# Kernel optimization log

Measured on AMD Instinct MI355X. Metric: run time of the kernel, lower is better.

Reference implementation:

```python
import jax, jax.numpy as jnp
import numpy as np

B, N_OCR, N_OBJ, D, H, L, DFF = 64, 64, 192, 768, 12, 4, 2048
DH = D // H
EPS = 1e-5  # torch LayerNorm default


def _ln(x, g, b):
    m = jnp.mean(x, axis=-1, keepdims=True)
    v = jnp.mean(jnp.square(x - m), axis=-1, keepdims=True)
    return (x - m) * jax.lax.rsqrt(v + EPS) * g + b


def setup_inputs():
    key = jax.random.key(0)
    ks = iter(jax.random.split(key, 32))
    s = 0.02
    f = lambda shape: jax.random.normal(next(ks), shape, jnp.float32) * s
    return {
        "ocr_feats": jax.random.normal(next(ks), (B, N_OCR, D), jnp.float32),
        "obj_feats": jax.random.normal(next(ks), (B, N_OBJ, D), jnp.float32),
        "ocr_dvs": jax.random.uniform(next(ks), (B, N_OCR, 1), jnp.float32, 0.1, 2.0),
        "obj_dvs": jax.random.uniform(next(ks), (B, N_OBJ, 1), jnp.float32, 0.1, 2.0),
        # SemanticAttentionDeFUM projections
        "sa_wq": f((D, D)), "sa_bq": jnp.zeros((D,), jnp.float32),
        "sa_wk": f((D, D)), "sa_bk": jnp.zeros((D,), jnp.float32),
        "sa_wv": f((D, D)), "sa_bv": jnp.zeros((D,), jnp.float32),
        # outer LayerNorm
        "ln0_g": jnp.ones((D,), jnp.float32), "ln0_b": jnp.zeros((D,), jnp.float32),
        # stacked TransformerEncoder layer params (post-norm, batch_first)
        "qkv_w": f((L, 3 * D, D)), "qkv_b": jnp.zeros((L, 3 * D), jnp.float32),
        "out_w": f((L, D, D)), "out_b": jnp.zeros((L, D), jnp.float32),
        "ln1_g": jnp.ones((L, D), jnp.float32), "ln1_b": jnp.zeros((L, D), jnp.float32),
        "ff1_w": f((L, DFF, D)), "ff1_b": jnp.zeros((L, DFF), jnp.float32),
        "ff2_w": f((L, D, DFF)), "ff2_b": jnp.zeros((L, D), jnp.float32),
        "ln2_g": jnp.ones((L, D), jnp.float32), "ln2_b": jnp.zeros((L, D), jnp.float32),
    }


def reference(ocr_feats, obj_feats, ocr_dvs, obj_dvs,
              sa_wq, sa_bq, sa_wk, sa_bk, sa_wv, sa_bv,
              ln0_g, ln0_b,
              qkv_w, qkv_b, out_w, out_b, ln1_g, ln1_b,
              ff1_w, ff1_b, ff2_w, ff2_b, ln2_g, ln2_b):
    num_ocr = ocr_feats.shape[1]
    x = jnp.concatenate([ocr_feats, obj_feats], axis=1)       # B,N,D
    dv = jnp.concatenate([ocr_dvs, obj_dvs], axis=1)[..., 0]  # B,N
    # vectorized cal_relative_depth_map: log(max(dv_i,dv_j)/min(dv_i,dv_j))
    R = jnp.log(jnp.maximum(dv[:, :, None], dv[:, None, :]) /
                jnp.minimum(dv[:, :, None], dv[:, None, :]))  # B,N,N
    # semantic attention: scores A and values V
    q = jnp.einsum('bnd,ed->bne', x, sa_wq) + sa_bq
    k = jnp.einsum('bnd,ed->bne', x, sa_wk) + sa_bk
    v = jnp.einsum('bnd,ed->bne', x, sa_wv) + sa_bv
    A = jnp.einsum('bqd,bkd->bqk', q, k) / jnp.sqrt(jnp.float32(D))
    att = jax.nn.softmax(A + R, axis=-1)
    h = _ln(x + jnp.einsum('bqk,bkd->bqd', att, v), ln0_g, ln0_b)

    def layer(h, p):
        qw, qb, ow, ob, l1g, l1b, f1w, f1b, f2w, f2b, l2g, l2b = p
        Bn, N, _ = h.shape
        qkv = jnp.einsum('bnd,ed->bne', h, qw) + qb            # B,N,3D
        qh, kh, vh = jnp.split(qkv, 3, axis=-1)
        qh = qh.reshape(Bn, N, H, DH).transpose(0, 2, 1, 3)
        kh = kh.reshape(Bn, N, H, DH).transpose(0, 2, 1, 3)
        vh = vh.reshape(Bn, N, H, DH).transpose(0, 2, 1, 3)
        sc = jnp.einsum('bhqd,bhkd->bhqk', qh, kh) / jnp.sqrt(jnp.float32(DH))
        o = jnp.einsum('bhqk,bhkd->bhqd', jax.nn.softmax(sc, axis=-1), vh)
        o = o.transpose(0, 2, 1, 3).reshape(Bn, N, D)
        o = jnp.einsum('bnd,ed->bne', o, ow) + ob
        h = _ln(h + o, l1g, l1b)
        ff = jnp.einsum('bnd,fd->bnf', h, f1w) + f1b
        ff = jax.nn.gelu(ff, approximate=False)  # torch 'gelu' = exact erf gelu
        ff = jnp.einsum('bnf,df->bnd', ff, f2w) + f2b
        h = _ln(h + ff, l2g, l2b)
        return h, None

    h, _ = jax.lax.scan(layer, h, (qkv_w, qkv_b, out_w, out_b,
                                   ln1_g, ln1_b, ff1_w, ff1_b,
                                   ff2_w, ff2_b, ln2_g, ln2_b))
    return h[:, :num_ocr, :]
```

## Files before the change

kernel.cpp:

```cpp
#include <hip/hip_runtime.h>

typedef unsigned short u16;
typedef __bf16 bf16_t;
typedef bf16_t bf16x8 __attribute__((ext_vector_type(8)));
typedef float f32x4 __attribute__((ext_vector_type(4)));
typedef unsigned int u32x4 __attribute__((ext_vector_type(4)));
typedef u16 u16x4 __attribute__((ext_vector_type(4)));

#define GL_LDS16(gp, lp)                                              \
  __builtin_amdgcn_global_load_lds(                                   \
      (const __attribute__((address_space(1))) void*)(gp),            \
      (__attribute__((address_space(3))) void*)(lp), 16, 0, 0)

__device__ __forceinline__ u16 f2bf(float f) {
  unsigned u = __builtin_bit_cast(unsigned, f);
  u += 0x7fff + ((u >> 16) & 1);
  return (u16)(u >> 16);
}
__device__ __forceinline__ float bf2f(u16 h) {
  unsigned u = ((unsigned)h) << 16;
  return __builtin_bit_cast(float, u);
}
__device__ __forceinline__ float wredSum(float v) {
#pragma unroll
  for (int m = 32; m; m >>= 1) v += __shfl_xor(v, m);
  return v;
}

__global__ __launch_bounds__(512, 2) void gemm3r(
    const u16* __restrict__ A, const u16* __restrict__ B,
    const float* __restrict__ bias, u16* __restrict__ C,
    int K, int N, int gx, int act, int tstore) {
  extern __shared__ __align__(16) char sm[];
  const int tid = threadIdx.x;
  const int l = tid & 63, w = tid >> 6, lg = l >> 4, li = l & 15;
  const int wr = w >> 2, wc = w & 3;

  int bid = blockIdx.x;
  int G = gx >> 3;
  int xcd = bid & 7, loc = bid >> 3;
  int mt = xcd * G + (loc % G), nt = loc / G;

  const u16* Ab = A + (long)mt * 256 * K;
  const u16* Bb = B + (long)nt * 256 * K;

  const long saoff = (long)(tid >> 2) * K + (((tid & 3) ^ ((tid >> 3) & 3)) << 3);
  const long rowK128 = (long)128 * K;
  const int t16 = tid * 16;

#define STAGE_A3(bi_, kt_)                                             \
  do {                                                                 \
    const u16* gp_ = Ab + saoff + ((long)(kt_) << 5);                  \
    char* lb_ = sm + (bi_) * 32768;                                    \
    GL_LDS16(gp_, lb_ + t16);                                          \
    GL_LDS16(gp_ + rowK128, lb_ + 8192 + t16);                         \
  } while (0)
#define STAGE_B3(bi_, kt_)                                             \
  do {                                                                 \
    const u16* gp_ = Bb + saoff + ((long)(kt_) << 5);                  \
    char* lb_ = sm + (bi_) * 32768 + 16384;                            \
    GL_LDS16(gp_, lb_ + t16);                                          \
    GL_LDS16(gp_ + rowK128, lb_ + 8192 + t16);                         \
  } while (0)

#define VM8 asm volatile("s_waitcnt vmcnt(8)" ::: "memory")
#define VM4 asm volatile("s_waitcnt vmcnt(4)" ::: "memory")
#define VM0 asm volatile("s_waitcnt vmcnt(0)" ::: "memory")

  int aof[2][4], bof[4];
#pragma unroll
  for (int hi = 0; hi < 2; ++hi)
#pragma unroll
    for (int f = 0; f < 4; ++f) {
      int ra = wr * 128 + hi * 64 + f * 16 + li;
      aof[hi][f] = ra * 64 + ((lg ^ ((ra >> 1) & 3)) << 4);
    }
#pragma unroll
  for (int f = 0; f < 4; ++f) {
    int rb = wc * 64 + f * 16 + li;
    bof[f] = 16384 + rb * 64 + ((lg ^ ((rb >> 1) & 3)) << 4);
  }

  f32x4 acc[8][4] = {};

  const int NT = K >> 5;
  STAGE_B3(0, 0); STAGE_A3(0, 0);
  STAGE_B3(1, 1); STAGE_A3(1, 1);
  STAGE_B3(2, 2); STAGE_A3(2, 2);

  for (int s = 0; s < NT; ++s) {
    const int bi = s & 3, bi3 = (s + 3) & 3;
    const char* ab = sm + bi * 32768;
    if (s < NT - 2) VM8; else if (s == NT - 2) VM4; else VM0;
    __builtin_amdgcn_s_barrier();
    asm volatile("" ::: "memory");
    if (s <= NT - 4) STAGE_B3(bi3, s + 3);
    bf16x8 afr[4], bfr[4];
#pragma unroll
    for (int f = 0; f < 4; ++f) {
      afr[f] = __builtin_bit_cast(bf16x8, *(const u32x4*)(ab + aof[0][f]));
      bfr[f] = __builtin_bit_cast(bf16x8, *(const u32x4*)(ab + bof[f]));
    }
    __builtin_amdgcn_s_setprio(1);
#pragma unroll
    for (int fi = 0; fi < 4; ++fi)
#pragma unroll
      for (int fj = 0; fj < 4; ++fj)
        acc[fi][fj] = __builtin_amdgcn_mfma_f32_16x16x32_bf16(afr[fi], bfr[fj], acc[fi][fj], 0, 0, 0);
    __builtin_amdgcn_s_setprio(0);
    if (s <= NT - 4) STAGE_A3(bi3, s + 3);
    bf16x8 ag[4];
#pragma unroll
    for (int f = 0; f < 4; ++f)
      ag[f] = __builtin_bit_cast(bf16x8, *(const u32x4*)(ab + aof[1][f]));
    __builtin_amdgcn_s_setprio(1);
#pragma unroll
    for (int fi = 0; fi < 4; ++fi)
#pragma unroll
      for (int fj = 0; fj < 4; ++fj)
        acc[4 + fi][fj] = __builtin_amdgcn_mfma_f32_16x16x32_bf16(ag[fi], bfr[fj], acc[4 + fi][fj], 0, 0, 0);
    __builtin_amdgcn_s_setprio(0);
  }

  long row0 = (long)mt * 256 + wr * 128;
  int col0 = nt * 256 + wc * 64;
#pragma unroll
  for (int fi = 0; fi < 8; ++fi) {
#pragma unroll
    for (int fj = 0; fj < 4; ++fj) {
      int c = col0 + fj * 16 + li;
      float bv = bias ? bias[c] : 0.f;
#pragma unroll
      for (int r = 0; r < 4; ++r) {
        float v = acc[fi][fj][r] + bv;
        if (act) v = 0.5f * v * (1.f + erff(v * 0.70710678118f));
        long row = row0 + fi * 16 + lg * 4 + r;
        long idx = tstore ? ((row >> 8) * 196608 + (long)c * 256 + (row & 255))
                          : (row * (long)N + c);
        C[idx] = f2bf(v);
      }
    }
  }
#undef STAGE_A3
#undef STAGE_B3
#undef VM8
#undef VM4
#undef VM0
}

__global__ __launch_bounds__(256) void gemm_bt(
    const u16* __restrict__ A, const u16* __restrict__ B,
    const float* __restrict__ bias, const float* __restrict__ logdv,
    float* __restrict__ Cf, u16* __restrict__ Cb,
    int K, int ldc, long sA, long sB, long sC, float alpha, int act, int tstore) {
  __shared__ __align__(16) u16 As[2][128 * 32];
  __shared__ __align__(16) u16 Bs[2][128 * 32];
  int tid = threadIdx.x, w = tid >> 6, l = tid & 63, lg = l >> 4, li = l & 15;
  int wr = w >> 1, wc = w & 1;
  long bz = blockIdx.z;
  const u16* Ab = A + bz * sA + (long)blockIdx.x * 128 * K;
  const u16* Bb = B + bz * sB + (long)blockIdx.y * 128 * K;

  int sr = tid >> 2, ss = tid & 3;
  long ga0 = (long)sr * K + ((ss ^ ((sr >> 1) & 3)) << 3);
  long gstep = (long)K << 6;

  int aoff[4], boff[4];
#pragma unroll
  for (int i = 0; i < 4; ++i) {
    int ra = wr * 64 + i * 16 + li;
    aoff[i] = ra * 64 + ((lg ^ ((ra >> 1) & 3)) << 4);
    int rb = wc * 64 + i * 16 + li;
    boff[i] = rb * 64 + ((lg ^ ((rb >> 1) & 3)) << 4);
  }

  f32x4 acc[4][4] = {};
  int wb = w * 1024;

  GL_LDS16(Ab + ga0, (char*)As + wb);
  GL_LDS16(Ab + ga0 + gstep, (char*)As + 4096 + wb);
  GL_LDS16(Bb + ga0, (char*)Bs + wb);
  GL_LDS16(Bb + ga0 + gstep, (char*)Bs + 4096 + wb);
  __syncthreads();

  int T = K >> 5;
  int bsel = 0;
  for (int kt = 0; kt < T; ++kt) {
    if (kt + 1 < T) {
      long ko = (long)(kt + 1) << 5;
      char* an = (char*)As + (bsel ^ 1) * 8192;
      char* bn = (char*)Bs + (bsel ^ 1) * 8192;
      GL_LDS16(Ab + ga0 + ko, an + wb);
      GL_LDS16(Ab + ga0 + gstep + ko, an + 4096 + wb);
      GL_LDS16(Bb + ga0 + ko, bn + wb);
      GL_LDS16(Bb + ga0 + gstep + ko, bn + 4096 + wb);
    }
    char* ac = (char*)As + bsel * 8192;
    char* bc = (char*)Bs + bsel * 8192;
    bf16x8 af[4], bq[4];
#pragma unroll
    for (int i = 0; i < 4; ++i) {
      af[i] = __builtin_bit_cast(bf16x8, *(const u32x4*)(ac + aoff[i]));
      bq[i] = __builtin_bit_cast(bf16x8, *(const u32x4*)(bc + boff[i]));
    }
#pragma unroll
    for (int i = 0; i < 4; ++i)
#pragma unroll
      for (int j = 0; j < 4; ++j)
        acc[i][j] = __builtin_amdgcn_mfma_f32_16x16x32_bf16(af[i], bq[j], acc[i][j], 0, 0, 0);
    __syncthreads();
    bsel ^= 1;
  }

  long row0 = (long)blockIdx.x * 128 + wr * 64;
  int col0 = blockIdx.y * 128 + wc * 64;
  float* cf = Cf ? Cf + bz * sC : (float*)0;
  u16* cb = Cb ? Cb + bz * sC : (u16*)0;
  const float* ldv = logdv ? logdv + bz * 256 : (const float*)0;
#pragma unroll
  for (int i = 0; i < 4; ++i) {
    long rb0 = row0 + i * 16 + lg * 4;
#pragma unroll
    for (int j = 0; j < 4; ++j) {
      int c = col0 + j * 16 + li;
      float bv = bias ? bias[c] : 0.f;
      float lj = ldv ? ldv[c] : 0.f;
#pragma unroll
      for (int r = 0; r < 4; ++r) {
        float v = acc[i][j][r] * alpha + bv;
        if (ldv) v += fabsf(ldv[rb0 + r] - lj);
        if (act) v = 0.5f * v * (1.f + erff(v * 0.70710678118f));
        long row = rb0 + r;
        long idx = tstore ? ((row >> 8) * 196608 + (long)c * 256 + (row & 255))
                          : (row * ldc + c);
        if (cf) cf[idx] = v;
        if (cb) cb[idx] = f2bf(v);
      }
    }
  }
}

__global__ __launch_bounds__(256) void mha_k(const u16* __restrict__ qkv, u16* __restrict__ obf) {
  __shared__ __align__(16) u16 Ks[256 * 64];
  __shared__ __align__(16) u16 Vt[64 * 256];
  int b = blockIdx.y;
  int h = blockIdx.x >> 2, qt = blockIdx.x & 3;
  int tid = threadIdx.x, w = tid >> 6, l = tid & 63, lg = l >> 4, li = l & 15;
  const u16* kb_ = qkv + (long)b * 256 * 2304 + 768 + h * 64;
  const u16* vb_ = qkv + (long)b * 256 * 2304 + 1536 + h * 64;
#pragma unroll
  for (int it = 0; it < 8; ++it) {
    int c = it * 256 + tid; int n = c >> 3, sl = c & 7;
    u32x4 d = *(const u32x4*)(kb_ + (long)n * 2304 + sl * 8);
    *(u32x4*)((char*)Ks + n * 128 + ((sl ^ (n & 7)) << 4)) = d;
  }
#pragma unroll
  for (int it = 0; it < 8; ++it) {
    int c = it * 256 + tid; int n = c >> 3, sl = c & 7;
    u32x4 dv = *(const u32x4*)(vb_ + (long)n * 2304 + sl * 8);
    const u16* pe = (const u16*)&dv;
#pragma unroll
    for (int j = 0; j < 8; ++j) {
      int dd = sl * 8 + j;
      *(u16*)((char*)Vt + dd * 512 + (((n >> 3) ^ (dd & 7)) << 4) + (n & 7) * 2) = pe[j];
    }
  }
  __syncthreads();

  long qrow = (long)b * 256 + qt * 64 + w * 16 + li;
  const u16* qp = qkv + qrow * 2304 + h * 64;
  bf16x8 qf0 = __builtin_bit_cast(bf16x8, *(const u32x4*)(qp + lg * 8));
  bf16x8 qf1 = __builtin_bit_cast(bf16x8, *(const u32x4*)(qp + 32 + lg * 8));

  f32x4 sacc[16] = {};
#pragma unroll
  for (int jt = 0; jt < 16; ++jt) {
    int j = jt * 16 + li;
    u32x4 k0 = *(const u32x4*)((char*)Ks + j * 128 + ((lg ^ (j & 7)) << 4));
    u32x4 k1 = *(const u32x4*)((char*)Ks + j * 128 + (((4 + lg) ^ (j & 7)) << 4));
    sacc[jt] = __builtin_amdgcn_mfma_f32_16x16x32_bf16(qf0, __builtin_bit_cast(bf16x8, k0), sacc[jt], 0, 0, 0);
    sacc[jt] = __builtin_amdgcn_mfma_f32_16x16x32_bf16(qf1, __builtin_bit_cast(bf16x8, k1), sacc[jt], 0, 0, 0);
  }
#pragma unroll
  for (int jt = 0; jt < 16; ++jt) sacc[jt] = sacc[jt] * 0.125f;

  float rinv[4];
#pragma unroll
  for (int r = 0; r < 4; ++r) {
    float m = -1e30f;
#pragma unroll
    for (int jt = 0; jt < 16; ++jt) m = fmaxf(m, sacc[jt][r]);
#pragma unroll
    for (int mk = 1; mk < 16; mk <<= 1) m = fmaxf(m, __shfl_xor(m, mk));
    float s = 0.f;
#pragma unroll
    for (int jt = 0; jt < 16; ++jt) { float e = __expf(sacc[jt][r] - m); sacc[jt][r] = e; s += e; }
#pragma unroll
    for (int mk = 1; mk < 16; mk <<= 1) s += __shfl_xor(s, mk);
    rinv[r] = 1.f / s;
  }
  __syncthreads();
  char* Ps = (char*)Ks + w * 8192;
#pragma unroll
  for (int jt = 0; jt < 16; ++jt) {
    int j = jt * 16 + li;
#pragma unroll
    for (int r = 0; r < 4; ++r) {
      int i = lg * 4 + r;
      *(u16*)(Ps + i * 512 + (((j >> 3) ^ (i & 7)) << 4) + (j & 7) * 2) = f2bf(sacc[jt][r]);
    }
  }
  __syncthreads();
  f32x4 oacc[4] = {};
#pragma unroll
  for (int kb2 = 0; kb2 < 8; ++kb2) {
    int sl = kb2 * 4 + lg;
    u32x4 pa = *(const u32x4*)(Ps + li * 512 + ((sl ^ (li & 7)) << 4));
#pragma unroll
    for (int dt = 0; dt < 4; ++dt) {
      int dd = dt * 16 + li;
      u32x4 vv = *(const u32x4*)((char*)Vt + dd * 512 + ((sl ^ (dd & 7)) << 4));
      oacc[dt] = __builtin_amdgcn_mfma_f32_16x16x32_bf16(__builtin_bit_cast(bf16x8, pa),
                                                         __builtin_bit_cast(bf16x8, vv), oacc[dt], 0, 0, 0);
    }
  }
  long orow = (long)b * 256 + qt * 64 + w * 16;
#pragma unroll
  for (int dt = 0; dt < 4; ++dt)
#pragma unroll
    for (int r = 0; r < 4; ++r) {
      float vvv = oacc[dt][r] * rinv[r];
      obf[(orow + lg * 4 + r) * 768 + h * 64 + dt * 16 + li] = f2bf(vvv);
    }
}

__global__ __launch_bounds__(256) void ln_k(const float* __restrict__ X, const u16* __restrict__ Rr,
                                            const float* __restrict__ g, const float* __restrict__ bb,
                                            float* __restrict__ oF, u16* __restrict__ oB) {
  long row = (long)blockIdx.x * 4 + (threadIdx.x >> 6);
  int l = threadIdx.x & 63;
  const float* x = X + row * 768;
  const u16* rr = Rr + row * 768;
  f32x4 v[3];
  float s = 0.f;
#pragma unroll
  for (int i = 0; i < 3; ++i) {
    f32x4 xv = *(const f32x4*)(x + i * 256 + l * 4);
    u16x4 rv = *(const u16x4*)(rr + i * 256 + l * 4);
#pragma unroll
    for (int j = 0; j < 4; ++j) xv[j] += bf2f(rv[j]);
    v[i] = xv;
    s += xv[0] + xv[1] + xv[2] + xv[3];
  }
  float mean = wredSum(s) * (1.f / 768.f);
  float q = 0.f;
#pragma unroll
  for (int i = 0; i < 3; ++i) {
#pragma unroll
    for (int j = 0; j < 4; ++j) { v[i][j] -= mean; q += v[i][j] * v[i][j]; }
  }
  float inv = rsqrtf(wredSum(q) * (1.f / 768.f) + 1e-5f);
#pragma unroll
  for (int i = 0; i < 3; ++i) {
    f32x4 gv = *(const f32x4*)(g + i * 256 + l * 4);
    f32x4 bv = *(const f32x4*)(bb + i * 256 + l * 4);
    f32x4 o;
    u16x4 ob;
#pragma unroll
    for (int j = 0; j < 4; ++j) { o[j] = v[i][j] * inv * gv[j] + bv[j]; ob[j] = f2bf(o[j]); }
    *(f32x4*)(oF + row * 768 + i * 256 + l * 4) = o;
    *(u16x4*)(oB + row * 768 + i * 256 + l * 4) = ob;
  }
}

__global__ __launch_bounds__(256) void smax_k(const float* __restrict__ S, u16* __restrict__ P) {
  long row = (long)blockIdx.x * 4 + (threadIdx.x >> 6);
  int l = threadIdx.x & 63;
  f32x4 v = *(const f32x4*)(S + row * 256 + l * 4);
  float m = fmaxf(fmaxf(v[0], v[1]), fmaxf(v[2], v[3]));
#pragma unroll
  for (int mk = 1; mk < 64; mk <<= 1) m = fmaxf(m, __shfl_xor(m, mk));
  float e0 = __expf(v[0] - m), e1 = __expf(v[1] - m), e2 = __expf(v[2] - m), e3 = __expf(v[3] - m);
  float s = wredSum(e0 + e1 + e2 + e3);
  float rn = 1.f / s;
  u16x4 o; o[0] = f2bf(e0 * rn); o[1] = f2bf(e1 * rn); o[2] = f2bf(e2 * rn); o[3] = f2bf(e3 * rn);
  *(u16x4*)(P + row * 256 + l * 4) = o;
}

__global__ __launch_bounds__(256) void conv_k(const float* __restrict__ in, u16* __restrict__ out, long n4) {
  long i = (long)blockIdx.x * 256 + threadIdx.x;
  if (i >= n4) return;
  f32x4 v = *(const f32x4*)(in + i * 4);
  u16x4 o; o[0] = f2bf(v[0]); o[1] = f2bf(v[1]); o[2] = f2bf(v[2]); o[3] = f2bf(v[3]);
  *(u16x4*)(out + i * 4) = o;
}

__global__ __launch_bounds__(256) void concat_k(const float* __restrict__ ocr, const float* __restrict__ obj,
                                                float* __restrict__ xf, u16* __restrict__ xb) {
  long i = (long)blockIdx.x * 256 + threadIdx.x;
  if (i >= 16384L * 192) return;
  long row = i / 192; int c4 = (int)(i % 192);
  int b = (int)(row >> 8), n = (int)(row & 255);
  const float* src = (n < 64) ? (ocr + ((long)(b * 64 + n)) * 768) : (obj + ((long)(b * 192 + n - 64)) * 768);
  f32x4 v = *(const f32x4*)(src + c4 * 4);
  *(f32x4*)(xf + row * 768 + c4 * 4) = v;
  u16x4 o; o[0] = f2bf(v[0]); o[1] = f2bf(v[1]); o[2] = f2bf(v[2]); o[3] = f2bf(v[3]);
  *(u16x4*)(xb + row * 768 + c4 * 4) = o;
}

__global__ __launch_bounds__(256) void logdv_k(const float* __restrict__ ocr_dv, const float* __restrict__ obj_dv,
                                               float* __restrict__ out) {
  int i = blockIdx.x * 256 + threadIdx.x;
  if (i >= 16384) return;
  int b = i >> 8, n = i & 255;
  float dv = (n < 64) ? ocr_dv[b * 64 + n] : obj_dv[b * 192 + n - 64];
  out[i] = logf(dv);
}

__global__ __launch_bounds__(256) void slice_k(const float* __restrict__ H, float* __restrict__ O) {
  long i = (long)blockIdx.x * 256 + threadIdx.x;
  if (i >= 786432) return;
  long idx = i * 4;
  long row = idx / 768; int c = (int)(idx % 768);
  long b = row >> 6, n = row & 63;
  *(f32x4*)(O + idx) = *(const f32x4*)(H + ((b * 256 + n) * 768 + c));
}

extern "C" void kernel_launch(void* const* d_in, const int* in_sizes, int n_in,
                              void* d_out, int out_size, void* d_ws, size_t ws_size,
                              hipStream_t stream) {
  const float* ocr = (const float*)d_in[0];
  const float* obj = (const float*)d_in[1];
  const float* ocr_dv = (const float*)d_in[2];
  const float* obj_dv = (const float*)d_in[3];
  const float* sa_wq = (const float*)d_in[4];
  const float* sa_bq = (const float*)d_in[5];
  const float* sa_wk = (const float*)d_in[6];
  const float* sa_bk = (const float*)d_in[7];
  const float* sa_wv = (const float*)d_in[8];
  const float* sa_bv = (const float*)d_in[9];
  const float* ln0_g = (const float*)d_in[10];
  const float* ln0_b = (const float*)d_in[11];
  const float* qkv_w = (const float*)d_in[12];
  const float* qkv_b = (const float*)d_in[13];
  const float* out_w = (const float*)d_in[14];
  const float* out_b = (const float*)d_in[15];
  const float* ln1_g = (const float*)d_in[16];
  const float* ln1_b = (const float*)d_in[17];
  const float* ff1_w = (const float*)d_in[18];
  const float* ff1_b = (const float*)d_in[19];
  const float* ff2_w = (const float*)d_in[20];
  const float* ff2_b = (const float*)d_in[21];
  const float* ln2_g = (const float*)d_in[22];
  const float* ln2_b = (const float*)d_in[23];

  (void)hipFuncSetAttribute((const void*)gemm3r,
                            hipFuncAttributeMaxDynamicSharedMemorySize, 131072);
  const unsigned DSM = 131072;

  char* ws = (char*)d_ws;
  float* XF = (float*)ws;
  u16* HB = (u16*)(ws + 50331648);
  float* LDV = (float*)(ws + 75497472);
  u16* WCV = (u16*)(ws + 75563008);
  char* SCR = ws + 86573056;

  const int bigws = ws_size >= (size_t)187236352;

  auto cv = [&](const float* src, long elems, u16* dst) {
    long n4 = elems >> 2;
    conv_k<<<dim3((unsigned)((n4 + 255) / 256)), dim3(256), 0, stream>>>(src, dst, n4);
  };

  concat_k<<<12288, 256, 0, stream>>>(ocr, obj, XF, HB);
  logdv_k<<<64, 256, 0, stream>>>(ocr_dv, obj_dv, LDV);

  const float SSC = 0.03608439182435161f;

  cv(sa_wq, 589824, WCV);
  cv(sa_wk, 589824, WCV + 589824);
  cv(sa_wv, 589824, WCV + 1179648);

  if (bigws) {
    u16* Qf = (u16*)SCR;
    u16* Kf = (u16*)(SCR + 25165824);
    u16* VTf = (u16*)(SCR + 50331648);
    float* Sfc = (float*)(SCR + 75497472);
    u16* Pc = (u16*)(SCR + 83886080);
    u16* ATTc = (u16*)(SCR + 88080384);
    gemm3r<<<192, 512, DSM, stream>>>(HB, WCV, sa_bq, Qf, 768, 768, 64, 0, 0);
    gemm3r<<<192, 512, DSM, stream>>>(HB, WCV + 589824, sa_bk, Kf, 768, 768, 64, 0, 0);
    gemm3r<<<192, 512, DSM, stream>>>(HB, WCV + 1179648, sa_bv, VTf, 768, 768, 64, 0, 1);
    for (int c = 0; c < 2; ++c) {
      long base = (long)c * 8192;
      gemm_bt<<<dim3(2, 2, 32), 256, 0, stream>>>(Qf + base * 768, Kf + base * 768, nullptr,
                                                  LDV + c * 8192, Sfc, nullptr, 768, 256,
                                                  196608, 196608, 65536, SSC, 0, 0);
      smax_k<<<2048, 256, 0, stream>>>(Sfc, Pc);
      gemm_bt<<<dim3(2, 6, 32), 256, 0, stream>>>(Pc, VTf + base * 768, nullptr, nullptr,
                                                  nullptr, ATTc, 256, 768, 65536, 196608, 196608, 1.f, 0, 0);
      ln_k<<<2048, 256, 0, stream>>>(XF + base * 768, ATTc, ln0_g, ln0_b, XF + base * 768, HB + base * 768);
    }
    u16* QKVf = (u16*)SCR;
    u16* Of = (u16*)(SCR + 75497472);
    u16* PRf = (u16*)SCR;
    u16* FFf = (u16*)(SCR + 25165824);
    for (int l = 0; l < 4; ++l) {
      cv(qkv_w + (long)l * 1769472, 1769472, WCV);
      cv(out_w + (long)l * 589824, 589824, WCV + 1769472);
      cv(ff1_w + (long)l * 1572864, 1572864, WCV + 2359296);
      cv(ff2_w + (long)l * 1572864, 1572864, WCV + 3932160);
      gemm3r<<<576, 512, DSM, stream>>>(HB, WCV, qkv_b + l * 2304, QKVf, 768, 2304, 64, 0, 0);
      mha_k<<<dim3(48, 64), 256, 0, stream>>>(QKVf, Of);
      gemm3r<<<192, 512, DSM, stream>>>(Of, WCV + 1769472, out_b + l * 768, PRf, 768, 768, 64, 0, 0);
      ln_k<<<4096, 256, 0, stream>>>(XF, PRf, ln1_g + l * 768, ln1_b + l * 768, XF, HB);
      gemm3r<<<512, 512, DSM, stream>>>(HB, WCV + 2359296, ff1_b + l * 2048, FFf, 768, 2048, 64, 1, 0);
      gemm3r<<<192, 512, DSM, stream>>>(FFf, WCV + 3932160, ff2_b + l * 768, PRf, 2048, 768, 64, 0, 0);
      ln_k<<<4096, 256, 0, stream>>>(XF, PRf, ln2_g + l * 768, ln2_b + l * 768, XF, HB);
    }
  } else {
    for (int c = 0; c < 2; ++c) {
      long base = (long)c * 8192;
      u16* Qc = (u16*)SCR;
      u16* Kc = (u16*)(SCR + 12582912);
      u16* VTc = (u16*)(SCR + 25165824);
      float* Sfc = (float*)(SCR + 37748736);
      u16* Pc = (u16*)(SCR + 46137344);
      u16* ATTc = (u16*)(SCR + 50331648);
      gemm3r<<<96, 512, DSM, stream>>>(HB + base * 768, WCV, sa_bq, Qc, 768, 768, 32, 0, 0);
      gemm3r<<<96, 512, DSM, stream>>>(HB + base * 768, WCV + 589824, sa_bk, Kc, 768, 768, 32, 0, 0);
      gemm3r<<<96, 512, DSM, stream>>>(HB + base * 768, WCV + 1179648, sa_bv, VTc, 768, 768, 32, 0, 1);
      gemm_bt<<<dim3(2, 2, 32), 256, 0, stream>>>(Qc, Kc, nullptr, LDV + c * 8192,
                                                  Sfc, nullptr, 768, 256, 196608, 196608, 65536, SSC, 0, 0);
      smax_k<<<2048, 256, 0, stream>>>(Sfc, Pc);
      gemm_bt<<<dim3(2, 6, 32), 256, 0, stream>>>(Pc, VTc, nullptr, nullptr,
                                                  nullptr, ATTc, 256, 768, 65536, 196608, 196608, 1.f, 0, 0);
      ln_k<<<2048, 256, 0, stream>>>(XF + base * 768, ATTc, ln0_g, ln0_b, XF + base * 768, HB + base * 768);
    }
    for (int l = 0; l < 4; ++l) {
      cv(qkv_w + (long)l * 1769472, 1769472, WCV);
      cv(out_w + (long)l * 589824, 589824, WCV + 1769472);
      cv(ff1_w + (long)l * 1572864, 1572864, WCV + 2359296);
      cv(ff2_w + (long)l * 1572864, 1572864, WCV + 3932160);
      for (int c = 0; c < 2; ++c) {
        long base = (long)c * 8192;
        u16* QKVc = (u16*)SCR;
        u16* Oc = (u16*)(SCR + 37748736);
        u16* PRc = (u16*)(SCR + 50331648);
        u16* FFc = (u16*)SCR;
        gemm3r<<<288, 512, DSM, stream>>>(HB + base * 768, WCV, qkv_b + l * 2304, QKVc, 768, 2304, 32, 0, 0);
        mha_k<<<dim3(48, 32), 256, 0, stream>>>(QKVc, Oc);
        gemm3r<<<96, 512, DSM, stream>>>(Oc, WCV + 1769472, out_b + l * 768, PRc, 768, 768, 32, 0, 0);
        ln_k<<<2048, 256, 0, stream>>>(XF + base * 768, PRc, ln1_g + l * 768, ln1_b + l * 768,
                                       XF + base * 768, HB + base * 768);
        gemm3r<<<256, 512, DSM, stream>>>(HB + base * 768, WCV + 2359296, ff1_b + l * 2048, FFc, 768, 2048, 32, 1, 0);
        gemm3r<<<96, 512, DSM, stream>>>(FFc, WCV + 3932160, ff2_b + l * 768, PRc, 2048, 768, 32, 0, 0);
        ln_k<<<2048, 256, 0, stream>>>(XF + base * 768, PRc, ln2_g + l * 768, ln2_b + l * 768,
                                       XF + base * 768, HB + base * 768);
      }
    }
  }
  slice_k<<<3072, 256, 0, stream>>>(XF, (float*)d_out);
}
```

Before: 1.965 ms.

## Shrink gemm3r block tile to 128x256 with 4 waves and 3-stage ring

Reworks the main GEMM kernel from 512-thread blocks with 256x256 tiles to 256-thread blocks with 128x256 tiles. Each wave still computes a 128x64 sub-tile. The 4-buffer prefetch ring becomes a 3-buffer ring with a single combined stage macro, and LDS drops from 128KB to 72KB. All launches double their grid sizes. The intent is more blocks for better CU occupancy and load balance on small-M GEMMs, at the cost of less B-tile reuse per block and a shallower prefetch depth.

```diff
diff --git a/kernel.cpp b/kernel.cpp
--- a/kernel.cpp
+++ b/kernel.cpp
@@ -27,44 +27,40 @@
   return v;
 }
 
-__global__ __launch_bounds__(512, 2) void gemm3r(
+__global__ __launch_bounds__(256, 2) void gemm3r(
     const u16* __restrict__ A, const u16* __restrict__ B,
     const float* __restrict__ bias, u16* __restrict__ C,
     int K, int N, int gx, int act, int tstore) {
   extern __shared__ __align__(16) char sm[];
   const int tid = threadIdx.x;
-  const int l = tid & 63, w = tid >> 6, lg = l >> 4, li = l & 15;
-  const int wr = w >> 2, wc = w & 3;
+  const int l = tid & 63, wc = tid >> 6, lg = l >> 4, li = l & 15;
 
   int bid = blockIdx.x;
   int G = gx >> 3;
   int xcd = bid & 7, loc = bid >> 3;
   int mt = xcd * G + (loc % G), nt = loc / G;
 
-  const u16* Ab = A + (long)mt * 256 * K;
+  const u16* Ab = A + (long)mt * 128 * K;
   const u16* Bb = B + (long)nt * 256 * K;
 
   const long saoff = (long)(tid >> 2) * K + (((tid & 3) ^ ((tid >> 3) & 3)) << 3);
-  const long rowK128 = (long)128 * K;
+  const long rowK64 = (long)64 * K;
   const int t16 = tid * 16;
 
-#define STAGE_A3(bi_, kt_)                                             \
+#define STAGE(bi_, kt_)                                                \
   do {                                                                 \
-    const u16* gp_ = Ab + saoff + ((long)(kt_) << 5);                  \
-    char* lb_ = sm + (bi_) * 32768;                                    \
-    GL_LDS16(gp_, lb_ + t16);                                          \
-    GL_LDS16(gp_ + rowK128, lb_ + 8192 + t16);                         \
+    char* lb_ = sm + (bi_) * 24576;                                    \
+    const u16* gb_ = Bb + saoff + ((long)(kt_) << 5);                  \
+    GL_LDS16(gb_, lb_ + 8192 + t16);                                   \
+    GL_LDS16(gb_ + rowK64, lb_ + 12288 + t16);                         \
+    GL_LDS16(gb_ + 2 * rowK64, lb_ + 16384 + t16);                     \
+    GL_LDS16(gb_ + 3 * rowK64, lb_ + 20480 + t16);                     \
+    const u16* ga_ = Ab + saoff + ((long)(kt_) << 5);                  \
+    GL_LDS16(ga_, lb_ + t16);                                          \
+    GL_LDS16(ga_ + rowK64, lb_ + 4096 + t16);                          \
   } while (0)
-#define STAGE_B3(bi_, kt_)                                             \
-  do {                                                                 \
-    const u16* gp_ = Bb + saoff + ((long)(kt_) << 5);                  \
-    char* lb_ = sm + (bi_) * 32768 + 16384;                            \
-    GL_LDS16(gp_, lb_ + t16);                                          \
-    GL_LDS16(gp_ + rowK128, lb_ + 8192 + t16);                         \
-  } while (0)
-
-#define VM8 asm volatile("s_waitcnt vmcnt(8)" ::: "memory")
-#define VM4 asm volatile("s_waitcnt vmcnt(4)" ::: "memory")
+
+#define VM6 asm volatile("s_waitcnt vmcnt(6)" ::: "memory")
 #define VM0 asm volatile("s_waitcnt vmcnt(0)" ::: "memory")
 
   int aof[2][4], bof[4];
@@ -72,34 +68,33 @@
   for (int hi = 0; hi < 2; ++hi)
 #pragma unroll
     for (int f = 0; f < 4; ++f) {
-      int ra = wr * 128 + hi * 64 + f * 16 + li;
+      int ra = hi * 64 + f * 16 + li;
       aof[hi][f] = ra * 64 + ((lg ^ ((ra >> 1) & 3)) << 4);
     }
 #pragma unroll
   for (int f = 0; f < 4; ++f) {
     int rb = wc * 64 + f * 16 + li;
-    bof[f] = 16384 + rb * 64 + ((lg ^ ((rb >> 1) & 3)) << 4);
+    bof[f] = 8192 + rb * 64 + ((lg ^ ((rb >> 1) & 3)) << 4);
   }
 
   f32x4 acc[8][4] = {};
 
   const int NT = K >> 5;
-  STAGE_B3(0, 0); STAGE_A3(0, 0);
-  STAGE_B3(1, 1); STAGE_A3(1, 1);
-  STAGE_B3(2, 2); STAGE_A3(2, 2);
+  STAGE(0, 0); STAGE(1, 1);
 
   for (int s = 0; s < NT; ++s) {
-    const int bi = s & 3, bi3 = (s + 3) & 3;
-    const char* ab = sm + bi * 32768;
-    if (s < NT - 2) VM8; else if (s == NT - 2) VM4; else VM0;
+    const int bi = s % 3;
+    const char* ab = sm + bi * 24576;
+    if (s == NT - 1) VM0; else VM6;
     __builtin_amdgcn_s_barrier();
     asm volatile("" ::: "memory");
-    if (s <= NT - 4) STAGE_B3(bi3, s + 3);
-    bf16x8 afr[4], bfr[4];
+    if (s + 2 < NT) { int b2 = (s + 2) % 3; STAGE(b2, s + 2); }
+    bf16x8 afr[4], bfr[4], ag[4];
 #pragma unroll
     for (int f = 0; f < 4; ++f) {
       afr[f] = __builtin_bit_cast(bf16x8, *(const u32x4*)(ab + aof[0][f]));
       bfr[f] = __builtin_bit_cast(bf16x8, *(const u32x4*)(ab + bof[f]));
+      ag[f]  = __builtin_bit_cast(bf16x8, *(const u32x4*)(ab + aof[1][f]));
     }
     __builtin_amdgcn_s_setprio(1);
 #pragma unroll
@@ -107,13 +102,6 @@
 #pragma unroll
       for (int fj = 0; fj < 4; ++fj)
         acc[fi][fj] = __builtin_amdgcn_mfma_f32_16x16x32_bf16(afr[fi], bfr[fj], acc[fi][fj], 0, 0, 0);
-    __builtin_amdgcn_s_setprio(0);
-    if (s <= NT - 4) STAGE_A3(bi3, s + 3);
-    bf16x8 ag[4];
-#pragma unroll
-    for (int f = 0; f < 4; ++f)
-      ag[f] = __builtin_bit_cast(bf16x8, *(const u32x4*)(ab + aof[1][f]));
-    __builtin_amdgcn_s_setprio(1);
 #pragma unroll
     for (int fi = 0; fi < 4; ++fi)
 #pragma unroll
@@ -122,7 +110,7 @@
     __builtin_amdgcn_s_setprio(0);
   }
 
-  long row0 = (long)mt * 256 + wr * 128;
+  long row0 = (long)mt * 128;
   int col0 = nt * 256 + wc * 64;
 #pragma unroll
   for (int fi = 0; fi < 8; ++fi) {
@@ -141,10 +129,8 @@
       }
     }
   }
-#undef STAGE_A3
-#undef STAGE_B3
-#undef VM8
-#undef VM4
+#undef STAGE
+#undef VM6
 #undef VM0
 }
 
@@ -455,8 +441,8 @@
   const float* ln2_b = (const float*)d_in[23];
 
   (void)hipFuncSetAttribute((const void*)gemm3r,
-                            hipFuncAttributeMaxDynamicSharedMemorySize, 131072);
-  const unsigned DSM = 131072;
+                            hipFuncAttributeMaxDynamicSharedMemorySize, 73728);
+  const unsigned DSM = 73728;
 
   char* ws = (char*)d_ws;
   float* XF = (float*)ws;
@@ -488,9 +474,9 @@
     float* Sfc = (float*)(SCR + 75497472);
     u16* Pc = (u16*)(SCR + 83886080);
     u16* ATTc = (u16*)(SCR + 88080384);
-    gemm3r<<<192, 512, DSM, stream>>>(HB, WCV, sa_bq, Qf, 768, 768, 64, 0, 0);
-    gemm3r<<<192, 512, DSM, stream>>>(HB, WCV + 589824, sa_bk, Kf, 768, 768, 64, 0, 0);
-    gemm3r<<<192, 512, DSM, stream>>>(HB, WCV + 1179648, sa_bv, VTf, 768, 768, 64, 0, 1);
+    gemm3r<<<384, 256, DSM, stream>>>(HB, WCV, sa_bq, Qf, 768, 768, 128, 0, 0);
+    gemm3r<<<384, 256, DSM, stream>>>(HB, WCV + 589824, sa_bk, Kf, 768, 768, 128, 0, 0);
+    gemm3r<<<384, 256, DSM, stream>>>(HB, WCV + 1179648, sa_bv, VTf, 768, 768, 128, 0, 1);
     for (int c = 0; c < 2; ++c) {
       long base = (long)c * 8192;
       gemm_bt<<<dim3(2, 2, 32), 256, 0, stream>>>(Qf + base * 768, Kf + base * 768, nullptr,
@@ -510,12 +496,12 @@
       cv(out_w + (long)l * 589824, 589824, WCV + 1769472);
       cv(ff1_w + (long)l * 1572864, 1572864, WCV + 2359296);
       cv(ff2_w + (long)l * 1572864, 1572864, WCV + 3932160);
-      gemm3r<<<576, 512, DSM, stream>>>(HB, WCV, qkv_b + l * 2304, QKVf, 768, 2304, 64, 0, 0);
+      gemm3r<<<1152, 256, DSM, stream>>>(HB, WCV, qkv_b + l * 2304, QKVf, 768, 2304, 128, 0, 0);
       mha_k<<<dim3(48, 64), 256, 0, stream>>>(QKVf, Of);
-      gemm3r<<<192, 512, DSM, stream>>>(Of, WCV + 1769472, out_b + l * 768, PRf, 768, 768, 64, 0, 0);
+      gemm3r<<<384, 256, DSM, stream>>>(Of, WCV + 1769472, out_b + l * 768, PRf, 768, 768, 128, 0, 0);
       ln_k<<<4096, 256, 0, stream>>>(XF, PRf, ln1_g + l * 768, ln1_b + l * 768, XF, HB);
-      gemm3r<<<512, 512, DSM, stream>>>(HB, WCV + 2359296, ff1_b + l * 2048, FFf, 768, 2048, 64, 1, 0);
-      gemm3r<<<192, 512, DSM, stream>>>(FFf, WCV + 3932160, ff2_b + l * 768, PRf, 2048, 768, 64, 0, 0);
+      gemm3r<<<1024, 256, DSM, stream>>>(HB, WCV + 2359296, ff1_b + l * 2048, FFf, 768, 2048, 128, 1, 0);
+      gemm3r<<<384, 256, DSM, stream>>>(FFf, WCV + 3932160, ff2_b + l * 768, PRf, 2048, 768, 128, 0, 0);
       ln_k<<<4096, 256, 0, stream>>>(XF, PRf, ln2_g + l * 768, ln2_b + l * 768, XF, HB);
     }
   } else {
@@ -527,9 +513,9 @@
       float* Sfc = (float*)(SCR + 37748736);
       u16* Pc = (u16*)(SCR + 46137344);
       u16* ATTc = (u16*)(SCR + 50331648);
-      gemm3r<<<96, 512, DSM, stream>>>(HB + base * 768, WCV, sa_bq, Qc, 768, 768, 32, 0, 0);
-      gemm3r<<<96, 512, DSM, stream>>>(HB + base * 768, WCV + 589824, sa_bk, Kc, 768, 768, 32, 0, 0);
-      gemm3r<<<96, 512, DSM, stream>>>(HB + base * 768, WCV + 1179648, sa_bv, VTc, 768, 768, 32, 0, 1);
+      gemm3r<<<192, 256, DSM, stream>>>(HB + base * 768, WCV, sa_bq, Qc, 768, 768, 64, 0, 0);
+      gemm3r<<<192, 256, DSM, stream>>>(HB + base * 768, WCV + 589824, sa_bk, Kc, 768, 768, 64, 0, 0);
+      gemm3r<<<192, 256, DSM, stream>>>(HB + base * 768, WCV + 1179648, sa_bv, VTc, 768, 768, 64, 0, 1);
       gemm_bt<<<dim3(2, 2, 32), 256, 0, stream>>>(Qc, Kc, nullptr, LDV + c * 8192,
                                                   Sfc, nullptr, 768, 256, 196608, 196608, 65536, SSC, 0, 0);
       smax_k<<<2048, 256, 0, stream>>>(Sfc, Pc);
@@ -548,13 +534,13 @@
         u16* Oc = (u16*)(SCR + 37748736);
         u16* PRc = (u16*)(SCR + 50331648);
         u16* FFc = (u16*)SCR;
-        gemm3r<<<288, 512, DSM, stream>>>(HB + base * 768, WCV, qkv_b + l * 2304, QKVc, 768, 2304, 32, 0, 0);
+        gemm3r<<<576, 256, DSM, stream>>>(HB + base * 768, WCV, qkv_b + l * 2304, QKVc, 768, 2304, 64, 0, 0);
         mha_k<<<dim3(48, 32), 256, 0, stream>>>(QKVc, Oc);
-        gemm3r<<<96, 512, DSM, stream>>>(Oc, WCV + 1769472, out_b + l * 768, PRc, 768, 768, 32, 0, 0);
+        gemm3r<<<192, 256, DSM, stream>>>(Oc, WCV + 1769472, out_b + l * 768, PRc, 768, 768, 64, 0, 0);
         ln_k<<<2048, 256, 0, stream>>>(XF + base * 768, PRc, ln1_g + l * 768, ln1_b + l * 768,
                                        XF + base * 768, HB + base * 768);
-        gemm3r<<<256, 512, DSM, stream>>>(HB + base * 768, WCV + 2359296, ff1_b + l * 2048, FFc, 768, 2048, 32, 1, 0);
-        gemm3r<<<96, 512, DSM, stream>>>(FFc, WCV + 3932160, ff2_b + l * 768, PRc, 2048, 768, 32, 0, 0);
+        gemm3r<<<512, 256, DSM, stream>>>(HB + base * 768, WCV + 2359296, ff1_b + l * 2048, FFc, 768, 2048, 64, 1, 0);
+        gemm3r<<<192, 256, DSM, stream>>>(FFc, WCV + 3932160, ff2_b + l * 768, PRc, 2048, 768, 64, 0, 0);
         ln_k<<<2048, 256, 0, stream>>>(XF + base * 768, PRc, ln2_g + l * 768, ln2_b + l * 768,
                                        XF + base * 768, HB + base * 768);
       }
```

Measured after the change: 1.952 ms. No clear change (-0.7%).

## Rewrite GEMM main loop as double-buffered 64-wide K ping-pong pipeline

Applied to the files above, without the earlier changes.

Replaces the 4-stage, 32-wide-K ring buffer GEMM with a 2-buffer scheme that loads 64 K-elements per stage, split into two 32-wide halves. Each half's MFMA block is bracketed by barriers, in the style of a ping-pong schedule that interleaves LDS reads with matrix-core work across waves. Launch bounds change from 2 to 1 block per CU. The intent is fewer pipeline waits per K step and better overlap of loads with MFMA. The cost is more barriers, lower occupancy and a shallower prefetch depth.

```diff
diff --git a/kernel.cpp b/kernel.cpp
--- a/kernel.cpp
+++ b/kernel.cpp
@@ -26,8 +26,11 @@
   for (int m = 32; m; m >>= 1) v += __shfl_xor(v, m);
   return v;
 }
-
-__global__ __launch_bounds__(512, 2) void gemm3r(
+__device__ __forceinline__ bf16x8 ldfrag(const char* p) {
+  return __builtin_bit_cast(bf16x8, *(const u32x4*)p);
+}
+
+__global__ __launch_bounds__(512, 1) void gemm8p(
     const u16* __restrict__ A, const u16* __restrict__ B,
     const float* __restrict__ bias, u16* __restrict__ C,
     int K, int N, int gx, int act, int tstore) {
@@ -44,82 +47,97 @@
   const u16* Ab = A + (long)mt * 256 * K;
   const u16* Bb = B + (long)nt * 256 * K;
 
-  const long saoff = (long)(tid >> 2) * K + (((tid & 3) ^ ((tid >> 3) & 3)) << 3);
-  const long rowK128 = (long)128 * K;
+  const long sa0 = (long)(tid >> 2) * K + (((tid & 3) ^ ((tid >> 3) & 3)) << 3);
+  const long K128 = (long)128 * K;
   const int t16 = tid * 16;
 
-#define STAGE_A3(bi_, kt_)                                             \
-  do {                                                                 \
-    const u16* gp_ = Ab + saoff + ((long)(kt_) << 5);                  \
-    char* lb_ = sm + (bi_) * 32768;                                    \
-    GL_LDS16(gp_, lb_ + t16);                                          \
-    GL_LDS16(gp_ + rowK128, lb_ + 8192 + t16);                         \
+#define STG(bi_, mat_, ks_, kt_)                                          \
+  do {                                                                    \
+    const u16* g_ = ((mat_) ? Bb : Ab) + sa0 + ((long)(kt_) << 6) + ((ks_) << 5); \
+    char* lb_ = sm + (bi_) * 65536 + (mat_) * 32768 + (ks_) * 16384;      \
+    GL_LDS16(g_, lb_ + t16);                                              \
+    GL_LDS16(g_ + K128, lb_ + 8192 + t16);                                \
   } while (0)
-#define STAGE_B3(bi_, kt_)                                             \
-  do {                                                                 \
-    const u16* gp_ = Bb + saoff + ((long)(kt_) << 5);                  \
-    char* lb_ = sm + (bi_) * 32768 + 16384;                            \
-    GL_LDS16(gp_, lb_ + t16);                                          \
-    GL_LDS16(gp_ + rowK128, lb_ + 8192 + t16);                         \
-  } while (0)
-
-#define VM8 asm volatile("s_waitcnt vmcnt(8)" ::: "memory")
+
 #define VM4 asm volatile("s_waitcnt vmcnt(4)" ::: "memory")
 #define VM0 asm volatile("s_waitcnt vmcnt(0)" ::: "memory")
-
-  int aof[2][4], bof[4];
-#pragma unroll
-  for (int hi = 0; hi < 2; ++hi)
-#pragma unroll
-    for (int f = 0; f < 4; ++f) {
-      int ra = wr * 128 + hi * 64 + f * 16 + li;
-      aof[hi][f] = ra * 64 + ((lg ^ ((ra >> 1) & 3)) << 4);
-    }
+#define BAR do { __builtin_amdgcn_s_barrier(); asm volatile("" ::: "memory"); } while (0)
+#define MFMA16(lo_, af_)                                                  \
+  do {                                                                    \
+    __builtin_amdgcn_s_setprio(1);                                        \
+    _Pragma("unroll") for (int fi_ = 0; fi_ < 4; ++fi_)                   \
+        _Pragma("unroll") for (int fj_ = 0; fj_ < 4; ++fj_)               \
+            acc[(lo_) + fi_][fj_] = __builtin_amdgcn_mfma_f32_16x16x32_bf16( \
+                (af_)[fi_], bfr[fj_], acc[(lo_) + fi_][fj_], 0, 0, 0);    \
+    __builtin_amdgcn_s_setprio(0);                                        \
+  } while (0)
+
+  int aof[8], bof[4];
+#pragma unroll
+  for (int f = 0; f < 8; ++f) {
+    int r = wr * 128 + f * 16 + li;
+    aof[f] = (r * 4 + (lg ^ ((r >> 1) & 3))) * 16;
+  }
 #pragma unroll
   for (int f = 0; f < 4; ++f) {
-    int rb = wc * 64 + f * 16 + li;
-    bof[f] = 16384 + rb * 64 + ((lg ^ ((rb >> 1) & 3)) << 4);
+    int r = wc * 64 + f * 16 + li;
+    bof[f] = 32768 + (r * 4 + (lg ^ ((r >> 1) & 3))) * 16;
   }
 
   f32x4 acc[8][4] = {};
-
-  const int NT = K >> 5;
-  STAGE_B3(0, 0); STAGE_A3(0, 0);
-  STAGE_B3(1, 1); STAGE_A3(1, 1);
-  STAGE_B3(2, 2); STAGE_A3(2, 2);
-
-  for (int s = 0; s < NT; ++s) {
-    const int bi = s & 3, bi3 = (s + 3) & 3;
-    const char* ab = sm + bi * 32768;
-    if (s < NT - 2) VM8; else if (s == NT - 2) VM4; else VM0;
-    __builtin_amdgcn_s_barrier();
-    asm volatile("" ::: "memory");
-    if (s <= NT - 4) STAGE_B3(bi3, s + 3);
-    bf16x8 afr[4], bfr[4];
-#pragma unroll
-    for (int f = 0; f < 4; ++f) {
-      afr[f] = __builtin_bit_cast(bf16x8, *(const u32x4*)(ab + aof[0][f]));
-      bfr[f] = __builtin_bit_cast(bf16x8, *(const u32x4*)(ab + bof[f]));
-    }
-    __builtin_amdgcn_s_setprio(1);
-#pragma unroll
-    for (int fi = 0; fi < 4; ++fi)
-#pragma unroll
-      for (int fj = 0; fj < 4; ++fj)
-        acc[fi][fj] = __builtin_amdgcn_mfma_f32_16x16x32_bf16(afr[fi], bfr[fj], acc[fi][fj], 0, 0, 0);
-    __builtin_amdgcn_s_setprio(0);
-    if (s <= NT - 4) STAGE_A3(bi3, s + 3);
-    bf16x8 ag[4];
-#pragma unroll
-    for (int f = 0; f < 4; ++f)
-      ag[f] = __builtin_bit_cast(bf16x8, *(const u32x4*)(ab + aof[1][f]));
-    __builtin_amdgcn_s_setprio(1);
-#pragma unroll
-    for (int fi = 0; fi < 4; ++fi)
-#pragma unroll
-      for (int fj = 0; fj < 4; ++fj)
-        acc[4 + fi][fj] = __builtin_amdgcn_mfma_f32_16x16x32_bf16(ag[fi], bfr[fj], acc[4 + fi][fj], 0, 0, 0);
-    __builtin_amdgcn_s_setprio(0);
+  bf16x8 bfr[4];
+
+  const int NT = K >> 6;
+  STG(0, 0, 0, 0); STG(0, 1, 0, 0);
+  STG(0, 0, 1, 0); STG(0, 1, 1, 0);
+  VM4; BAR;
+
+  for (int t = 0; t < NT; ++t) {
+    const int bi = t & 1, b2 = bi ^ 1;
+    const char* ab0 = sm + bi * 65536;
+    const char* ab1 = ab0 + 16384;
+    if (t + 1 < NT) { STG(b2, 0, 0, t + 1); STG(b2, 1, 0, t + 1); }
+    {
+      bf16x8 afr[4];
+#pragma unroll
+      for (int f = 0; f < 4; ++f) {
+        afr[f] = ldfrag(ab0 + aof[f]);
+        bfr[f] = ldfrag(ab0 + bof[f]);
+      }
+      BAR;
+      MFMA16(0, afr);
+      BAR;
+    }
+    if (t == NT - 1) VM0; else VM4;
+    if (t + 1 < NT) { STG(b2, 0, 1, t + 1); STG(b2, 1, 1, t + 1); }
+    {
+      bf16x8 afr[4];
+#pragma unroll
+      for (int f = 0; f < 4; ++f) afr[f] = ldfrag(ab0 + aof[4 + f]);
+      BAR;
+      MFMA16(4, afr);
+      BAR;
+    }
+    {
+      bf16x8 afr[4];
+#pragma unroll
+      for (int f = 0; f < 4; ++f) {
+        afr[f] = ldfrag(ab1 + aof[f]);
+        bfr[f] = ldfrag(ab1 + bof[f]);
+      }
+      BAR;
+      MFMA16(0, afr);
+      BAR;
+    }
+    VM4;
+    {
+      bf16x8 afr[4];
+#pragma unroll
+      for (int f = 0; f < 4; ++f) afr[f] = ldfrag(ab1 + aof[4 + f]);
+      BAR;
+      MFMA16(4, afr);
+      BAR;
+    }
   }
 
   long row0 = (long)mt * 256 + wr * 128;
@@ -141,11 +159,11 @@
       }
     }
   }
-#undef STAGE_A3
-#undef STAGE_B3
-#undef VM8
+#undef STG
 #undef VM4
 #undef VM0
+#undef BAR
+#undef MFMA16
 }
 
 __global__ __launch_bounds__(256) void gemm_bt(
@@ -454,7 +472,7 @@
   const float* ln2_g = (const float*)d_in[22];
   const float* ln2_b = (const float*)d_in[23];
 
-  (void)hipFuncSetAttribute((const void*)gemm3r,
+  (void)hipFuncSetAttribute((const void*)gemm8p,
                             hipFuncAttributeMaxDynamicSharedMemorySize, 131072);
   const unsigned DSM = 131072;
 
@@ -488,9 +506,9 @@
     float* Sfc = (float*)(SCR + 75497472);
     u16* Pc = (u16*)(SCR + 83886080);
     u16* ATTc = (u16*)(SCR + 88080384);
-    gemm3r<<<192, 512, DSM, stream>>>(HB, WCV, sa_bq, Qf, 768, 768, 64, 0, 0);
-    gemm3r<<<192, 512, DSM, stream>>>(HB, WCV + 589824, sa_bk, Kf, 768, 768, 64, 0, 0);
-    gemm3r<<<192, 512, DSM, stream>>>(HB, WCV + 1179648, sa_bv, VTf, 768, 768, 64, 0, 1);
+    gemm8p<<<192, 512, DSM, stream>>>(HB, WCV, sa_bq, Qf, 768, 768, 64, 0, 0);
+    gemm8p<<<192, 512, DSM, stream>>>(HB, WCV + 589824, sa_bk, Kf, 768, 768, 64, 0, 0);
+    gemm8p<<<192, 512, DSM, stream>>>(HB, WCV + 1179648, sa_bv, VTf, 768, 768, 64, 0, 1);
     for (int c = 0; c < 2; ++c) {
       long base = (long)c * 8192;
       gemm_bt<<<dim3(2, 2, 32), 256, 0, stream>>>(Qf + base * 768, Kf + base * 768, nullptr,
@@ -510,12 +528,12 @@
       cv(out_w + (long)l * 589824, 589824, WCV + 1769472);
       cv(ff1_w + (long)l * 1572864, 1572864, WCV + 2359296);
       cv(ff2_w + (long)l * 1572864, 1572864, WCV + 3932160);
-      gemm3r<<<576, 512, DSM, stream>>>(HB, WCV, qkv_b + l * 2304, QKVf, 768, 2304, 64, 0, 0);
+      gemm8p<<<576, 512, DSM, stream>>>(HB, WCV, qkv_b + l * 2304, QKVf, 768, 2304, 64, 0, 0);
       mha_k<<<dim3(48, 64), 256, 0, stream>>>(QKVf, Of);
-      gemm3r<<<192, 512, DSM, stream>>>(Of, WCV + 1769472, out_b + l * 768, PRf, 768, 768, 64, 0, 0);
+      gemm8p<<<192, 512, DSM, stream>>>(Of, WCV + 1769472, out_b + l * 768, PRf, 768, 768, 64, 0, 0);
       ln_k<<<4096, 256, 0, stream>>>(XF, PRf, ln1_g + l * 768, ln1_b + l * 768, XF, HB);
-      gemm3r<<<512, 512, DSM, stream>>>(HB, WCV + 2359296, ff1_b + l * 2048, FFf, 768, 2048, 64, 1, 0);
-      gemm3r<<<192, 512, DSM, stream>>>(FFf, WCV + 3932160, ff2_b + l * 768, PRf, 2048, 768, 64, 0, 0);
+      gemm8p<<<512, 512, DSM, stream>>>(HB, WCV + 2359296, ff1_b + l * 2048, FFf, 768, 2048, 64, 1, 0);
+      gemm8p<<<192, 512, DSM, stream>>>(FFf, WCV + 3932160, ff2_b + l * 768, PRf, 2048, 768, 64, 0, 0);
       ln_k<<<4096, 256, 0, stream>>>(XF, PRf, ln2_g + l * 768, ln2_b + l * 768, XF, HB);
     }
   } else {
@@ -527,9 +545,9 @@
       float* Sfc = (float*)(SCR + 37748736);
       u16* Pc = (u16*)(SCR + 46137344);
       u16* ATTc = (u16*)(SCR + 50331648);
-      gemm3r<<<96, 512, DSM, stream>>>(HB + base * 768, WCV, sa_bq, Qc, 768, 768, 32, 0, 0);
-      gemm3r<<<96, 512, DSM, stream>>>(HB + base * 768, WCV + 589824, sa_bk, Kc, 768, 768, 32, 0, 0);
-      gemm3r<<<96, 512, DSM, stream>>>(HB + base * 768, WCV + 1179648, sa_bv, VTc, 768, 768, 32, 0, 1);
+      gemm8p<<<96, 512, DSM, stream>>>(HB + base * 768, WCV, sa_bq, Qc, 768, 768, 32, 0, 0);
+      gemm8p<<<96, 512, DSM, stream>>>(HB + base * 768, WCV + 589824, sa_bk, Kc, 768, 768, 32, 0, 0);
+      gemm8p<<<96, 512, DSM, stream>>>(HB + base * 768, WCV + 1179648, sa_bv, VTc, 768, 768, 32, 0, 1);
       gemm_bt<<<dim3(2, 2, 32), 256, 0, stream>>>(Qc, Kc, nullptr, LDV + c * 8192,
                                                   Sfc, nullptr, 768, 256, 196608, 196608, 65536, SSC, 0, 0);
       smax_k<<<2048, 256, 0, stream>>>(Sfc, Pc);
@@ -548,13 +566,13 @@
         u16* Oc = (u16*)(SCR + 37748736);
         u16* PRc = (u16*)(SCR + 50331648);
         u16* FFc = (u16*)SCR;
-        gemm3r<<<288, 512, DSM, stream>>>(HB + base * 768, WCV, qkv_b + l * 2304, QKVc, 768, 2304, 32, 0, 0);
+        gemm8p<<<288, 512, DSM, stream>>>(HB + base * 768, WCV, qkv_b + l * 2304, QKVc, 768, 2304, 32, 0, 0);
         mha_k<<<dim3(48, 32), 256, 0, stream>>>(QKVc, Oc);
-        gemm3r<<<96, 512, DSM, stream>>>(Oc, WCV + 1769472, out_b + l * 768, PRc, 768, 768, 32, 0, 0);
+        gemm8p<<<96, 512, DSM, stream>>>(Oc, WCV + 1769472, out_b + l * 768, PRc, 768, 768, 32, 0, 0);
         ln_k<<<2048, 256, 0, stream>>>(XF + base * 768, PRc, ln1_g + l * 768, ln1_b + l * 768,
                                        XF + base * 768, HB + base * 768);
-        gemm3r<<<256, 512, DSM, stream>>>(HB + base * 768, WCV + 2359296, ff1_b + l * 2048, FFc, 768, 2048, 32, 1, 0);
-        gemm3r<<<96, 512, DSM, stream>>>(FFc, WCV + 3932160, ff2_b + l * 768, PRc, 2048, 768, 32, 0, 0);
+        gemm8p<<<256, 512, DSM, stream>>>(HB + base * 768, WCV + 2359296, ff1_b + l * 2048, FFc, 768, 2048, 32, 1, 0);
+        gemm8p<<<96, 512, DSM, stream>>>(FFc, WCV + 3932160, ff2_b + l * 768, PRc, 2048, 768, 32, 0, 0);
         ln_k<<<2048, 256, 0, stream>>>(XF + base * 768, PRc, ln2_g + l * 768, ln2_b + l * 768,
                                        XF + base * 768, HB + base * 768);
       }
```

New measurement: 2.055 ms. 1.05x slower.
